# Kernel optimization log

Hardware: AMD Instinct MI355X
Metric: run time of the kernel (lower is better)

The kernel has to match this reference:

```python
import jax, jax.numpy as jnp
import numpy as np

B, C, H, W = 32, 256, 56, 56
KS, NK = 7, 16
EPS = 1e-5

def setup_inputs() -> dict:
    key = jax.random.key(0)
    ks = jax.random.split(key, 9)
    return {
        "x": jax.random.normal(ks[0], (B, C, H, W), jnp.float32),
        "bn_gamma": jax.random.normal(ks[1], (C,), jnp.float32) * 0.1 + 1.0,
        "bn_beta": jax.random.normal(ks[2], (C,), jnp.float32) * 0.1,
        "bn_mean": jax.random.normal(ks[3], (C,), jnp.float32) * 0.1,
        "bn_var": jax.random.uniform(ks[4], (C,), jnp.float32) + 0.5,
        "q_w": jax.random.normal(ks[5], (C, C), jnp.float32) / np.sqrt(C),
        "k_w": jax.random.normal(ks[6], (NK, C), jnp.float32) / np.sqrt(C),
        "kernel_bank": jax.random.normal(ks[7], (NK, KS * KS), jnp.float32),
        "bias": jnp.zeros((C,), jnp.float32),
    }

def reference(x, bn_gamma, bn_beta, bn_mean, bn_var, q_w, k_w, kernel_bank, bias):
    b, c, h, w = x.shape
    temp = 2.0 * c  # self.temp = channels * 2
    # BatchNorm2d (eval mode: affine with running stats)
    scale = bn_gamma / jnp.sqrt(bn_var + EPS)
    xn = (x - bn_mean[:, None, None]) * scale[:, None, None] + bn_beta[:, None, None]
    xf = xn.reshape(b, c, h * w)                       # [B, C, HW]
    Q = jnp.einsum('oc,bcn->bon', q_w, xf)             # 1x1 conv -> [B, C, HW]
    K = jnp.einsum('kc,bcn->bnk', k_w, xf)             # 1x1 conv -> [B, HW, NK]
    attn = jax.nn.softmax(jnp.einsum('bcn,bnk->bck', Q, K) / temp, axis=2)  # [B, C, NK]
    wgt = jnp.einsum('bck,ke->bce', attn, kernel_bank)  # [B, C, KS*KS]
    wgt = wgt.reshape(b * c, 1, KS, KS)                # per-sample per-channel kernels
    pad = KS // 2
    # dynamic depthwise conv: groups = B*C  (torch padding='same')
    out = jax.lax.conv_general_dilated(
        x.reshape(1, b * c, h, w), wgt,
        window_strides=(1, 1), padding=[(pad, pad), (pad, pad)],
        feature_group_count=b * c,
        dimension_numbers=('NCHW', 'OIHW', 'NCHW'))
    return out.reshape(b, c, h, w) + bias[None, :, None, None]
```

## Files before the change

### kernel.cpp

```cpp
#include <hip/hip_runtime.h>

#define BATCH 32
#define CH    256
#define HWPX  3136
#define WIDTH 56
#define NK    16
#define NSLAB 28
#define NSUB  4
#define WGTS  52
#define EPSV  1e-5f

__global__ __launch_bounds__(64) void kkvec(
    const float* __restrict__ x,
    const float* __restrict__ gamma, const float* __restrict__ beta,
    const float* __restrict__ mean,  const float* __restrict__ var,
    const float* __restrict__ kw,    float* __restrict__ Kpart)
{
    const int sub = blockIdx.x / 784;
    const int pb  = blockIdx.x % 784;
    const int job = pb * 64 + threadIdx.x;
    const int b   = job / 1568;
    const int px2 = job % 1568;
    const int cbase = sub * 64;
    const float* xp = x + ((size_t)b * CH + cbase) * HWPX + px2 * 2;

    float acc0[NK], acc1[NK];
#pragma unroll
    for (int k = 0; k < NK; ++k) { acc0[k] = 0.f; acc1[k] = 0.f; }

    for (int c0 = 0; c0 < 64; c0 += 8) {
        float2 v[8];
#pragma unroll
        for (int i = 0; i < 8; ++i)
            v[i] = *(const float2*)(xp + (size_t)(c0 + i) * HWPX);
#pragma unroll
        for (int i = 0; i < 8; ++i) {
            const int c = cbase + c0 + i;
            const float sc = gamma[c] * rsqrtf(var[c] + EPSV);
            const float sh = fmaf(-mean[c], sc, beta[c]);
            v[i].x = fmaf(v[i].x, sc, sh);
            v[i].y = fmaf(v[i].y, sc, sh);
        }
#pragma unroll
        for (int k = 0; k < NK; ++k) {
            const float4 w0 = *(const float4*)(kw + k * CH + cbase + c0);
            const float4 w1 = *(const float4*)(kw + k * CH + cbase + c0 + 4);
            acc0[k] = fmaf(v[0].x, w0.x, acc0[k]); acc1[k] = fmaf(v[0].y, w0.x, acc1[k]);
            acc0[k] = fmaf(v[1].x, w0.y, acc0[k]); acc1[k] = fmaf(v[1].y, w0.y, acc1[k]);
            acc0[k] = fmaf(v[2].x, w0.z, acc0[k]); acc1[k] = fmaf(v[2].y, w0.z, acc1[k]);
            acc0[k] = fmaf(v[3].x, w0.w, acc0[k]); acc1[k] = fmaf(v[3].y, w0.w, acc1[k]);
            acc0[k] = fmaf(v[4].x, w1.x, acc0[k]); acc1[k] = fmaf(v[4].y, w1.x, acc1[k]);
            acc0[k] = fmaf(v[5].x, w1.y, acc0[k]); acc1[k] = fmaf(v[5].y, w1.y, acc1[k]);
            acc0[k] = fmaf(v[6].x, w1.z, acc0[k]); acc1[k] = fmaf(v[6].y, w1.z, acc1[k]);
            acc0[k] = fmaf(v[7].x, w1.w, acc0[k]); acc1[k] = fmaf(v[7].y, w1.w, acc1[k]);
        }
    }

    float* op = Kpart + ((size_t)sub * BATCH * HWPX + (size_t)b * HWPX + px2 * 2) * NK;
#pragma unroll
    for (int kq = 0; kq < 4; ++kq)
        ((float4*)op)[kq] = make_float4(acc0[kq*4+0], acc0[kq*4+1], acc0[kq*4+2], acc0[kq*4+3]);
#pragma unroll
    for (int kq = 0; kq < 4; ++kq)
        ((float4*)op)[4+kq] = make_float4(acc1[kq*4+0], acc1[kq*4+1], acc1[kq*4+2], acc1[kq*4+3]);
}

__global__ __launch_bounds__(256) void ksum(
    const float* __restrict__ Kpart, float* __restrict__ Kbuf)
{
    const int i = blockIdx.x * 256 + threadIdx.x;
    const float4* p = (const float4*)Kpart;
    float4 s = p[i];
#pragma unroll
    for (int s2 = 1; s2 < NSUB; ++s2) {
        const float4 v = p[(size_t)s2 * 401408 + i];
        s.x += v.x; s.y += v.y; s.z += v.z; s.w += v.w;
    }
    ((float4*)Kbuf)[i] = s;
}

__global__ __launch_bounds__(256) void kpmat(
    const float* __restrict__ x,
    const float* __restrict__ gamma, const float* __restrict__ beta,
    const float* __restrict__ mean,  const float* __restrict__ var,
    const float* __restrict__ Kbuf,  float* __restrict__ Pp)
{
    const int b  = blockIdx.x / NSLAB;
    const int nb = blockIdx.x % NSLAB;
    const int n0 = nb * 112;
    const int c  = threadIdx.x;

    const float sc = gamma[c] * rsqrtf(var[c] + EPSV);
    const float sh = fmaf(-mean[c], sc, beta[c]);

    const float4* xr = (const float4*)(x + ((size_t)b * CH + c) * HWPX + n0);
    const float*  Kp = Kbuf + ((size_t)b * HWPX + n0) * NK;

    float acc[NK];
#pragma unroll
    for (int k = 0; k < NK; ++k) acc[k] = 0.f;

#pragma unroll 4
    for (int j = 0; j < 28; ++j) {
        const float4 xv = xr[j];
        float v[4];
        v[0] = fmaf(xv.x, sc, sh); v[1] = fmaf(xv.y, sc, sh);
        v[2] = fmaf(xv.z, sc, sh); v[3] = fmaf(xv.w, sc, sh);
#pragma unroll
        for (int d = 0; d < 4; ++d) {
            const float vd = v[d];
#pragma unroll
            for (int kq = 0; kq < 4; ++kq) {
                const float4 kv = *(const float4*)(Kp + ((j*4 + d) * NK) + kq*4);
                acc[kq*4+0] = fmaf(vd, kv.x, acc[kq*4+0]);
                acc[kq*4+1] = fmaf(vd, kv.y, acc[kq*4+1]);
                acc[kq*4+2] = fmaf(vd, kv.z, acc[kq*4+2]);
                acc[kq*4+3] = fmaf(vd, kv.w, acc[kq*4+3]);
            }
        }
    }
    float4* op = (float4*)(Pp + (((size_t)b * NSLAB + nb) * CH + c) * NK);
#pragma unroll
    for (int kq = 0; kq < 4; ++kq)
        op[kq] = make_float4(acc[kq*4+0], acc[kq*4+1], acc[kq*4+2], acc[kq*4+3]);
}

__global__ __launch_bounds__(256) void kpred(
    const float* __restrict__ Pp, float* __restrict__ P)
{
    const int idx = blockIdx.x * 256 + threadIdx.x;
    const int b = idx >> 12;
    const int e = idx & 4095;
    const float* p = Pp + (size_t)b * NSLAB * 4096 + e;
    float s = 0.f;
#pragma unroll
    for (int nb = 0; nb < NSLAB; ++nb) s += p[(size_t)nb * 4096];
    P[idx] = s;
}

__global__ __launch_bounds__(256) void ksoft(
    const float* __restrict__ P, const float* __restrict__ qw,
    const float* __restrict__ bank, float* __restrict__ wgt)
{
    const int b  = blockIdx.x >> 3;
    const int cb = blockIdx.x & 7;
    const int tid = threadIdx.x;

    __shared__ float s_P[CH * NK];
    __shared__ float s_red[32 * 8 * NK];
    __shared__ float s_S[32 * NK];
    __shared__ float s_attn[32 * NK];

    for (int idx = tid; idx < CH * NK; idx += 256)
        s_P[idx] = P[(size_t)b * CH * NK + idx];
    __syncthreads();

    const int c_l = tid & 31, sub = tid >> 5;
    const int c = cb * 32 + c_l;
    float a[NK];
#pragma unroll
    for (int k = 0; k < NK; ++k) a[k] = 0.f;
    const float* qrow = qw + (size_t)c * CH + sub * 32;
    for (int j = 0; j < 32; ++j) {
        const float qv = qrow[j];
        const float4* p4 = (const float4*)&s_P[(sub * 32 + j) * NK];
#pragma unroll
        for (int kq = 0; kq < 4; ++kq) {
            const float4 pv = p4[kq];
            a[kq*4+0] = fmaf(qv, pv.x, a[kq*4+0]);
            a[kq*4+1] = fmaf(qv, pv.y, a[kq*4+1]);
            a[kq*4+2] = fmaf(qv, pv.z, a[kq*4+2]);
            a[kq*4+3] = fmaf(qv, pv.w, a[kq*4+3]);
        }
    }
#pragma unroll
    for (int kq = 0; kq < 4; ++kq)
        *(float4*)&s_red[(c_l * 8 + sub) * NK + kq*4] =
            make_float4(a[kq*4+0], a[kq*4+1], a[kq*4+2], a[kq*4+3]);
    __syncthreads();

    for (int idx = tid; idx < 32 * NK; idx += 256) {
        const int cl = idx >> 4, k = idx & 15;
        float s = 0.f;
#pragma unroll
        for (int s2 = 0; s2 < 8; ++s2) s += s_red[(cl * 8 + s2) * NK + k];
        s_S[idx] = s * (1.f / 512.f);
    }
    __syncthreads();

    if (tid < 32) {
        float l[NK];
#pragma unroll
        for (int k = 0; k < NK; ++k) l[k] = s_S[tid * NK + k];
        float m = l[0];
#pragma unroll
        for (int k = 1; k < NK; ++k) m = fmaxf(m, l[k]);
        float sum = 0.f;
#pragma unroll
        for (int k = 0; k < NK; ++k) { l[k] = __expf(l[k] - m); sum += l[k]; }
        const float inv = 1.f / sum;
#pragma unroll
        for (int k = 0; k < NK; ++k) s_attn[tid * NK + k] = l[k] * inv;
    }
    __syncthreads();

    for (int idx = tid; idx < 32 * 49; idx += 256) {
        const int cl = idx / 49, e = idx - cl * 49;
        float wv = 0.f;
#pragma unroll
        for (int k = 0; k < NK; ++k)
            wv = fmaf(s_attn[cl * NK + k], bank[k * 49 + e], wv);
        wgt[((size_t)b * CH + cb * 32 + cl) * WGTS + e] = wv;
    }
}

__global__ __launch_bounds__(256) void kconv(
    const float* __restrict__ x, const float* __restrict__ wgt,
    const float* __restrict__ bias, float* __restrict__ out)
{
    const int t  = threadIdx.x;
    const int pl = t >> 4;
    const int q  = t & 15;
    const int qc = q < 14 ? q : 13;
    const int h  = blockIdx.x & 1;
    const int plane = (blockIdx.x >> 1) * 16 + pl;
    const int ho = h * 28;
    const bool qlo = (q == 0), qhi = (q >= 13);
    const float bv = bias[plane & 255];

    float4 wv[13];
    const float4* wp4 = (const float4*)(wgt + (size_t)plane * WGTS);
#pragma unroll
    for (int i = 0; i < 13; ++i) wv[i] = wp4[i];
#define WTAP(idx) ((idx)%4==0 ? wv[(idx)/4].x : (idx)%4==1 ? wv[(idx)/4].y : \
                   (idx)%4==2 ? wv[(idx)/4].z : wv[(idx)/4].w)

    const float* xrow = x   + (size_t)plane * HWPX + 4 * qc;
    float*       orow = out + (size_t)plane * HWPX + 4 * qc;

    float a[7][4];
#pragma unroll
    for (int i = 0; i < 7; ++i)
#pragma unroll
        for (int ix = 0; ix < 4; ++ix) a[i][ix] = bv;

    const float4 z4 = make_float4(0.f, 0.f, 0.f, 0.f);
    int ir0 = ho - 3;
    float4 vc = (0 <= ir0 && ir0 < 56) ? *(const float4*)(xrow + ir0 * WIDTH) : z4;

#pragma unroll 7
    for (int j = 0; j < 35; ++j) {
        const int snew = j % 7;
#pragma unroll
        for (int ix = 0; ix < 4; ++ix) a[snew][ix] = bv;

        const int irn = ho - 3 + j + 1;
        float4 vn = (0 <= irn && irn < 56 && j + 1 < 35)
                        ? *(const float4*)(xrow + irn * WIDTH) : z4;

        float rr1 = __shfl_up(vc.y, 1), rr2 = __shfl_up(vc.z, 1), rr3 = __shfl_up(vc.w, 1);
        float rr8 = __shfl_down(vc.x, 1), rr9 = __shfl_down(vc.y, 1), rr10 = __shfl_down(vc.z, 1);
        float rr[11];
        rr[1] = qlo ? 0.f : rr1;  rr[2] = qlo ? 0.f : rr2;  rr[3] = qlo ? 0.f : rr3;
        rr[4] = vc.x; rr[5] = vc.y; rr[6] = vc.z; rr[7] = vc.w;
        rr[8] = qhi ? 0.f : rr8;  rr[9] = qhi ? 0.f : rr9;  rr[10] = qhi ? 0.f : rr10;

#pragma unroll
        for (int i = 0; i < 7; ++i) {
            const int ky = 6 - i;
            const int s  = (j + i + 1) % 7;
#pragma unroll
            for (int kx = 0; kx < 7; ++kx) {
                const float wk = WTAP(ky * 7 + kx);
#pragma unroll
                for (int ix = 0; ix < 4; ++ix)
                    a[s][ix] = fmaf(wk, rr[ix + kx + 1], a[s][ix]);
            }
        }

        if (j >= 6 && j < 34) {
            const int o  = ho + j - 6;
            const int sd = (j + 1) % 7;
            if (q < 14)
                *(float4*)(orow + o * WIDTH) =
                    make_float4(a[sd][0], a[sd][1], a[sd][2], a[sd][3]);
        }
        vc = vn;
    }
#undef WTAP
}

extern "C" void kernel_launch(void* const* d_in, const int* in_sizes, int n_in,
                              void* d_out, int out_size, void* d_ws, size_t ws_size,
                              hipStream_t stream)
{
    const float* x     = (const float*)d_in[0];
    const float* gamma = (const float*)d_in[1];
    const float* beta  = (const float*)d_in[2];
    const float* mean  = (const float*)d_in[3];
    const float* var   = (const float*)d_in[4];
    const float* qw    = (const float*)d_in[5];
    const float* kw    = (const float*)d_in[6];
    const float* bank  = (const float*)d_in[7];
    const float* bias  = (const float*)d_in[8];
    float* out = (float*)d_out;

    float* ws    = (float*)d_ws;
    float* Kpart = ws;
    float* Pp    = ws;
    float* Kbuf  = ws + (size_t)NSUB * BATCH * HWPX * NK;
    float* P     = Kbuf + (size_t)BATCH * HWPX * NK;
    float* wgt   = P + (size_t)BATCH * CH * NK;

    kkvec<<<dim3(NSUB * 784),   dim3(64),  0, stream>>>(x, gamma, beta, mean, var, kw, Kpart);
    ksum <<<dim3(1568),         dim3(256), 0, stream>>>(Kpart, Kbuf);
    kpmat<<<dim3(BATCH * NSLAB),dim3(256), 0, stream>>>(x, gamma, beta, mean, var, Kbuf, Pp);
    kpred<<<dim3(512),          dim3(256), 0, stream>>>(Pp, P);
    ksoft<<<dim3(BATCH * 8),    dim3(256), 0, stream>>>(P, qw, bank, wgt);
    kconv<<<dim3(BATCH * CH / 8), dim3(256), 0, stream>>>(x, wgt, bias, out);
}
```

Before: 137.2 us.

## Fuse K projection, split reduction and P matmul into one tiled shared-memory kernel

Replaces the separate K-projection, partial-sum and P-matrix kernels with one kernel per (batch, 64-pixel tile). Each tile of normalized x is staged in shared memory, K for the tile is computed there, and the tile is immediately contracted against x to give partial P. This removes the large Kpart and Kbuf global round trips and a second read of x. The cost is more partial slabs for kpred to reduce (49 instead of 28) and about 70KB of LDS per block, which limits occupancy.

```diff
diff --git a/kernel.cpp b/kernel.cpp
--- a/kernel.cpp
+++ b/kernel.cpp
@@ -5,124 +5,93 @@
 #define HWPX  3136
 #define WIDTH 56
 #define NK    16
-#define NSLAB 28
-#define NSUB  4
+#define NT    49
 #define WGTS  52
 #define EPSV  1e-5f
 
-__global__ __launch_bounds__(64) void kkvec(
+__global__ __launch_bounds__(256) void kfuse(
     const float* __restrict__ x,
     const float* __restrict__ gamma, const float* __restrict__ beta,
     const float* __restrict__ mean,  const float* __restrict__ var,
-    const float* __restrict__ kw,    float* __restrict__ Kpart)
-{
-    const int sub = blockIdx.x / 784;
-    const int pb  = blockIdx.x % 784;
-    const int job = pb * 64 + threadIdx.x;
-    const int b   = job / 1568;
-    const int px2 = job % 1568;
-    const int cbase = sub * 64;
-    const float* xp = x + ((size_t)b * CH + cbase) * HWPX + px2 * 2;
-
-    float acc0[NK], acc1[NK];
-#pragma unroll
-    for (int k = 0; k < NK; ++k) { acc0[k] = 0.f; acc1[k] = 0.f; }
-
-    for (int c0 = 0; c0 < 64; c0 += 8) {
-        float2 v[8];
-#pragma unroll
-        for (int i = 0; i < 8; ++i)
-            v[i] = *(const float2*)(xp + (size_t)(c0 + i) * HWPX);
-#pragma unroll
-        for (int i = 0; i < 8; ++i) {
-            const int c = cbase + c0 + i;
-            const float sc = gamma[c] * rsqrtf(var[c] + EPSV);
-            const float sh = fmaf(-mean[c], sc, beta[c]);
-            v[i].x = fmaf(v[i].x, sc, sh);
-            v[i].y = fmaf(v[i].y, sc, sh);
-        }
-#pragma unroll
-        for (int k = 0; k < NK; ++k) {
-            const float4 w0 = *(const float4*)(kw + k * CH + cbase + c0);
-            const float4 w1 = *(const float4*)(kw + k * CH + cbase + c0 + 4);
-            acc0[k] = fmaf(v[0].x, w0.x, acc0[k]); acc1[k] = fmaf(v[0].y, w0.x, acc1[k]);
-            acc0[k] = fmaf(v[1].x, w0.y, acc0[k]); acc1[k] = fmaf(v[1].y, w0.y, acc1[k]);
-            acc0[k] = fmaf(v[2].x, w0.z, acc0[k]); acc1[k] = fmaf(v[2].y, w0.z, acc1[k]);
-            acc0[k] = fmaf(v[3].x, w0.w, acc0[k]); acc1[k] = fmaf(v[3].y, w0.w, acc1[k]);
-            acc0[k] = fmaf(v[4].x, w1.x, acc0[k]); acc1[k] = fmaf(v[4].y, w1.x, acc1[k]);
-            acc0[k] = fmaf(v[5].x, w1.y, acc0[k]); acc1[k] = fmaf(v[5].y, w1.y, acc1[k]);
-            acc0[k] = fmaf(v[6].x, w1.z, acc0[k]); acc1[k] = fmaf(v[6].y, w1.z, acc1[k]);
-            acc0[k] = fmaf(v[7].x, w1.w, acc0[k]); acc1[k] = fmaf(v[7].y, w1.w, acc1[k]);
-        }
-    }
-
-    float* op = Kpart + ((size_t)sub * BATCH * HWPX + (size_t)b * HWPX + px2 * 2) * NK;
-#pragma unroll
-    for (int kq = 0; kq < 4; ++kq)
-        ((float4*)op)[kq] = make_float4(acc0[kq*4+0], acc0[kq*4+1], acc0[kq*4+2], acc0[kq*4+3]);
-#pragma unroll
-    for (int kq = 0; kq < 4; ++kq)
-        ((float4*)op)[4+kq] = make_float4(acc1[kq*4+0], acc1[kq*4+1], acc1[kq*4+2], acc1[kq*4+3]);
-}
-
-__global__ __launch_bounds__(256) void ksum(
-    const float* __restrict__ Kpart, float* __restrict__ Kbuf)
-{
-    const int i = blockIdx.x * 256 + threadIdx.x;
-    const float4* p = (const float4*)Kpart;
-    float4 s = p[i];
-#pragma unroll
-    for (int s2 = 1; s2 < NSUB; ++s2) {
-        const float4 v = p[(size_t)s2 * 401408 + i];
-        s.x += v.x; s.y += v.y; s.z += v.z; s.w += v.w;
-    }
-    ((float4*)Kbuf)[i] = s;
-}
-
-__global__ __launch_bounds__(256) void kpmat(
-    const float* __restrict__ x,
-    const float* __restrict__ gamma, const float* __restrict__ beta,
-    const float* __restrict__ mean,  const float* __restrict__ var,
-    const float* __restrict__ Kbuf,  float* __restrict__ Pp)
-{
-    const int b  = blockIdx.x / NSLAB;
-    const int nb = blockIdx.x % NSLAB;
-    const int n0 = nb * 112;
-    const int c  = threadIdx.x;
-
-    const float sc = gamma[c] * rsqrtf(var[c] + EPSV);
-    const float sh = fmaf(-mean[c], sc, beta[c]);
-
-    const float4* xr = (const float4*)(x + ((size_t)b * CH + c) * HWPX + n0);
-    const float*  Kp = Kbuf + ((size_t)b * HWPX + n0) * NK;
-
-    float acc[NK];
-#pragma unroll
-    for (int k = 0; k < NK; ++k) acc[k] = 0.f;
-
+    const float* __restrict__ kw,    float* __restrict__ Pp)
+{
+    const int b   = blockIdx.x / NT;
+    const int t   = blockIdx.x % NT;
+    const int n0  = t * 64;
+    const int tid = threadIdx.x;
+
+    __shared__ float s_x[CH * 65];
+    __shared__ float s_K[NK * 64];
+
+    {
+        const int c = tid;
+        const float sc = gamma[c] * rsqrtf(var[c] + EPSV);
+        const float sh = fmaf(-mean[c], sc, beta[c]);
+        const float4* xr = (const float4*)(x + ((size_t)b * CH + c) * HWPX + n0);
+        float* dst = s_x + c * 65;
+#pragma unroll
+        for (int j = 0; j < 16; ++j) {
+            const float4 v = xr[j];
+            dst[4*j+0] = fmaf(v.x, sc, sh);
+            dst[4*j+1] = fmaf(v.y, sc, sh);
+            dst[4*j+2] = fmaf(v.z, sc, sh);
+            dst[4*j+3] = fmaf(v.w, sc, sh);
+        }
+    }
+    __syncthreads();
+
+    {
+        const int w = tid >> 6;
+        const int p = tid & 63;
+        float ka[4] = {0.f, 0.f, 0.f, 0.f};
 #pragma unroll 4
-    for (int j = 0; j < 28; ++j) {
-        const float4 xv = xr[j];
-        float v[4];
-        v[0] = fmaf(xv.x, sc, sh); v[1] = fmaf(xv.y, sc, sh);
-        v[2] = fmaf(xv.z, sc, sh); v[3] = fmaf(xv.w, sc, sh);
-#pragma unroll
-        for (int d = 0; d < 4; ++d) {
-            const float vd = v[d];
-#pragma unroll
-            for (int kq = 0; kq < 4; ++kq) {
-                const float4 kv = *(const float4*)(Kp + ((j*4 + d) * NK) + kq*4);
-                acc[kq*4+0] = fmaf(vd, kv.x, acc[kq*4+0]);
-                acc[kq*4+1] = fmaf(vd, kv.y, acc[kq*4+1]);
-                acc[kq*4+2] = fmaf(vd, kv.z, acc[kq*4+2]);
-                acc[kq*4+3] = fmaf(vd, kv.w, acc[kq*4+3]);
+        for (int c = 0; c < CH; c += 4) {
+            const float xv0 = s_x[(c+0)*65 + p];
+            const float xv1 = s_x[(c+1)*65 + p];
+            const float xv2 = s_x[(c+2)*65 + p];
+            const float xv3 = s_x[(c+3)*65 + p];
+#pragma unroll
+            for (int i = 0; i < 4; ++i) {
+                const float4 k4 = *(const float4*)(kw + (4*w+i)*CH + c);
+                ka[i] = fmaf(xv0, k4.x, ka[i]);
+                ka[i] = fmaf(xv1, k4.y, ka[i]);
+                ka[i] = fmaf(xv2, k4.z, ka[i]);
+                ka[i] = fmaf(xv3, k4.w, ka[i]);
             }
         }
-    }
-    float4* op = (float4*)(Pp + (((size_t)b * NSLAB + nb) * CH + c) * NK);
-#pragma unroll
-    for (int kq = 0; kq < 4; ++kq)
-        op[kq] = make_float4(acc[kq*4+0], acc[kq*4+1], acc[kq*4+2], acc[kq*4+3]);
+#pragma unroll
+        for (int i = 0; i < 4; ++i) s_K[(4*w+i)*64 + p] = ka[i];
+    }
+    __syncthreads();
+
+    {
+        const int c = tid;
+        float acc[NK];
+#pragma unroll
+        for (int k = 0; k < NK; ++k) acc[k] = 0.f;
+        const float* xrowp = s_x + c * 65;
+#pragma unroll
+        for (int j0 = 0; j0 < 64; j0 += 16) {
+            float xr_[16];
+#pragma unroll
+            for (int j = 0; j < 16; ++j) xr_[j] = xrowp[j0 + j];
+#pragma unroll
+            for (int k = 0; k < NK; ++k) {
+#pragma unroll
+                for (int q = 0; q < 4; ++q) {
+                    const float4 kv = *(const float4*)(s_K + k*64 + j0 + 4*q);
+                    acc[k] = fmaf(xr_[4*q+0], kv.x, acc[k]);
+                    acc[k] = fmaf(xr_[4*q+1], kv.y, acc[k]);
+                    acc[k] = fmaf(xr_[4*q+2], kv.z, acc[k]);
+                    acc[k] = fmaf(xr_[4*q+3], kv.w, acc[k]);
+                }
+            }
+        }
+        float* op = Pp + (((size_t)b * NT + t) * CH + c) * NK;
+#pragma unroll
+        for (int kq = 0; kq < 4; ++kq)
+            ((float4*)op)[kq] = make_float4(acc[kq*4+0], acc[kq*4+1], acc[kq*4+2], acc[kq*4+3]);
+    }
 }
 
 __global__ __launch_bounds__(256) void kpred(
@@ -131,10 +100,10 @@
     const int idx = blockIdx.x * 256 + threadIdx.x;
     const int b = idx >> 12;
     const int e = idx & 4095;
-    const float* p = Pp + (size_t)b * NSLAB * 4096 + e;
+    const float* p = Pp + (size_t)b * NT * 4096 + e;
     float s = 0.f;
 #pragma unroll
-    for (int nb = 0; nb < NSLAB; ++nb) s += p[(size_t)nb * 4096];
+    for (int t = 0; t < NT; ++t) s += p[(size_t)t * 4096];
     P[idx] = s;
 }
 
@@ -305,16 +274,12 @@
     const float* bias  = (const float*)d_in[8];
     float* out = (float*)d_out;
 
-    float* ws    = (float*)d_ws;
-    float* Kpart = ws;
-    float* Pp    = ws;
-    float* Kbuf  = ws + (size_t)NSUB * BATCH * HWPX * NK;
-    float* P     = Kbuf + (size_t)BATCH * HWPX * NK;
-    float* wgt   = P + (size_t)BATCH * CH * NK;
-
-    kkvec<<<dim3(NSUB * 784),   dim3(64),  0, stream>>>(x, gamma, beta, mean, var, kw, Kpart);
-    ksum <<<dim3(1568),         dim3(256), 0, stream>>>(Kpart, Kbuf);
-    kpmat<<<dim3(BATCH * NSLAB),dim3(256), 0, stream>>>(x, gamma, beta, mean, var, Kbuf, Pp);
+    float* ws  = (float*)d_ws;
+    float* Pp  = ws;
+    float* P   = Pp + (size_t)BATCH * NT * CH * NK;
+    float* wgt = P + (size_t)BATCH * CH * NK;
+
+    kfuse<<<dim3(BATCH * NT),   dim3(256), 0, stream>>>(x, gamma, beta, mean, var, kw, Pp);
     kpred<<<dim3(512),          dim3(256), 0, stream>>>(Pp, P);
     ksoft<<<dim3(BATCH * 8),    dim3(256), 0, stream>>>(P, qw, bank, wgt);
     kconv<<<dim3(BATCH * CH / 8), dim3(256), 0, stream>>>(x, wgt, bias, out);
```

Measured after the change: 158.4 us. 1.15x slower.
